# Performance work log

Measured on AMD Instinct MI355X. Metric: run time of the kernel, lower is better.

## Reference

```python
import jax, jax.numpy as jnp
import numpy as np

D_MODEL, D_INNER, D_STATE, D_CONV = 1024, 2048, 16, 4
LN_EPS = 1e-5


def setup_inputs() -> dict:
    key = jax.random.key(0)
    ks = jax.random.split(key, 8)
    B, T = 2, 1024
    s = 0.02
    A = jnp.broadcast_to(jnp.arange(1, D_STATE + 1, dtype=jnp.float32), (D_INNER, D_STATE))
    return {
        "x": jax.random.normal(ks[0], (B, T, D_MODEL), jnp.float32),
        "ln_gamma": jnp.ones((D_MODEL,), jnp.float32),
        "ln_beta": jnp.zeros((D_MODEL,), jnp.float32),
        "W_in": jax.random.normal(ks[1], (2 * D_INNER, D_MODEL), jnp.float32) * s,
        "conv_w": jax.random.normal(ks[2], (D_INNER, D_CONV), jnp.float32) * s,
        "conv_b": jnp.zeros((D_INNER,), jnp.float32),
        "W_x": jax.random.normal(ks[3], (2 * D_STATE + 1, D_INNER), jnp.float32) * s,
        "w_dt": jax.random.normal(ks[4], (D_INNER, 1), jnp.float32) * s,
        "b_dt": jnp.zeros((D_INNER,), jnp.float32),
        "A_log": jnp.log(A),
        "D_param": jnp.ones((D_INNER,), jnp.float32),
        "W_out": jax.random.normal(ks[5], (D_MODEL, D_INNER), jnp.float32) * s,
    }


def _mamba_forward(x, ln_gamma, ln_beta, W_in, conv_w, conv_b, W_x, w_dt, b_dt, A_log, D_param, W_out):
    residual = x
    B, T, _ = x.shape
    # LayerNorm
    mu = x.mean(-1, keepdims=True)
    var = ((x - mu) ** 2).mean(-1, keepdims=True)
    xn = (x - mu) / jnp.sqrt(var + LN_EPS) * ln_gamma + ln_beta
    # in_proj -> split into x branch and gate z
    xz = xn @ W_in.T                       # [B,T,2*d_inner]
    xb, z = jnp.split(xz, 2, axis=-1)
    # depthwise causal conv1d (torch pad=d_conv-1, truncated to T == left pad)
    xp = jnp.pad(xb, ((0, 0), (D_CONV - 1, 0), (0, 0)))
    xc = conv_b + sum(xp[:, k:k + T, :] * conv_w[:, k] for k in range(D_CONV))
    xc = jax.nn.silu(xc)                   # [B,T,d_inner]
    # ssm parameter projections
    ssm_p = xc @ W_x.T                     # [B,T,2*d_state+1]
    dt_raw = ssm_p[..., :1]
    Bp = ssm_p[..., 1:1 + D_STATE]
    Cp = ssm_p[..., 1 + D_STATE:]
    dt = jax.nn.softplus(dt_raw @ w_dt.T + b_dt)   # [B,T,d_inner]
    A = -jnp.exp(A_log)                    # [d_inner,d_state]

    def step(h, inp):
        dt_t, x_t, B_t, C_t = inp          # [B,d], [B,d], [B,n], [B,n]
        A_bar = jnp.exp(dt_t[:, :, None] * A[None])          # [B,d,n]
        h = A_bar * h + (dt_t * x_t)[:, :, None] * B_t[:, None, :]
        y_t = jnp.einsum('bdn,bn->bd', h, C_t)
        return h, y_t

    h0 = jnp.zeros((B, D_INNER, D_STATE), x.dtype)
    xs = (jnp.swapaxes(dt, 0, 1), jnp.swapaxes(xc, 0, 1),
          jnp.swapaxes(Bp, 0, 1), jnp.swapaxes(Cp, 0, 1))
    _, ys = jax.lax.scan(step, h0, xs)     # ys: [T,B,d_inner]
    y = jnp.swapaxes(ys, 0, 1)
    y = y + D_param * xc
    y = y * jax.nn.silu(z)
    return residual + y @ W_out.T


def reference(x, ln_gamma, ln_beta, W_in, conv_w, conv_b, W_x, w_dt, b_dt, A_log, D_param, W_out):
    return _mamba_forward(x, ln_gamma, ln_beta, W_in, conv_w, conv_b, W_x, w_dt, b_dt, A_log, D_param, W_out)
```

## Files before the change

### kernel.cpp

```cpp
#include <hip/hip_runtime.h>
#include <hip/hip_bf16.h>

#define DM 1024
#define DI 2048
#define DS 16
#define DC 4
#define BB 2
#define TT 1024
#define MM (BB*TT)
#define CCH 32
#define LCH 32
#define PR 8
#define REPS 2

typedef unsigned short u16;
typedef __attribute__((ext_vector_type(8))) short bf16x8;
typedef __attribute__((ext_vector_type(4))) float f32x4;

#if __has_builtin(__builtin_amdgcn_exp2f)
#define EXP2F(x) __builtin_amdgcn_exp2f(x)
#else
#define EXP2F(x) exp2f(x)
#endif
#define L2E 1.44269504f

__device__ __forceinline__ float bu2f(u16 u) {
    union { unsigned int i; float f; } w; w.i = ((unsigned int)u) << 16; return w.f;
}
__device__ __forceinline__ u16 f2bu(float f) {
    union { float f; unsigned int u; } w; w.f = f;
    unsigned int r = w.u + 0x7fffu + ((w.u >> 16) & 1u);
    return (u16)(r >> 16);
}
__device__ __forceinline__ float upk(const uint4& v, int e) {
    unsigned int u;
    switch (e >> 1) { case 0: u = v.x; break; case 1: u = v.y; break;
                      case 2: u = v.z; break; default: u = v.w; }
    union { unsigned int i; float f; } w;
    w.i = (e & 1) ? (u & 0xffff0000u) : (u << 16);
    return w.f;
}

#define F2B_BLOCKS 6210
__global__ __launch_bounds__(256) void prep_kernel(const float* __restrict__ x,
                                                   const float* __restrict__ gamma,
                                                   const float* __restrict__ beta,
                                                   u16* __restrict__ xn,
                                                   const float* __restrict__ Wi,
                                                   u16* __restrict__ Wi_b,
                                                   const float* __restrict__ Wo,
                                                   u16* __restrict__ Wo_b,
                                                   const float* __restrict__ Wx,
                                                   u16* __restrict__ Wx_b) {
    const int tid = threadIdx.x;
    if (blockIdx.x >= MM) {
        const int n4W  = 2 * DI * DM / 4;
        const int n4Wo = DM * DI / 4;
        int i = (blockIdx.x - MM) * 256 + tid;
        const float* in; u16* out;
        if (i < n4W) { in = Wi; out = Wi_b; }
        else if (i < n4W + n4Wo) { in = Wo; out = Wo_b; i -= n4W; }
        else { in = Wx; out = Wx_b; i -= n4W + n4Wo; }
        float4 v = reinterpret_cast<const float4*>(in)[i];
        ushort4 o;
        o.x = f2bu(v.x); o.y = f2bu(v.y); o.z = f2bu(v.z); o.w = f2bu(v.w);
        reinterpret_cast<ushort4*>(out)[i] = o;
        return;
    }
    __shared__ float sbuf[8];
    const int row = blockIdx.x;
    float4 v = reinterpret_cast<const float4*>(x + (size_t)row * DM)[tid];

    float s = v.x + v.y + v.z + v.w;
    #pragma unroll
    for (int off = 32; off; off >>= 1) s += __shfl_down(s, off);
    if ((tid & 63) == 0) sbuf[tid >> 6] = s;
    __syncthreads();
    float mu = (sbuf[0] + sbuf[1] + sbuf[2] + sbuf[3]) * (1.0f / DM);
    __syncthreads();

    float d0 = v.x - mu, d1 = v.y - mu, d2 = v.z - mu, d3 = v.w - mu;
    float q = d0*d0 + d1*d1 + d2*d2 + d3*d3;
    #pragma unroll
    for (int off = 32; off; off >>= 1) q += __shfl_down(q, off);
    if ((tid & 63) == 0) sbuf[tid >> 6] = q;
    __syncthreads();
    float var = (sbuf[0] + sbuf[1] + sbuf[2] + sbuf[3]) * (1.0f / DM);
    float rstd = rsqrtf(var + 1e-5f);

    float4 g = reinterpret_cast<const float4*>(gamma)[tid];
    float4 b = reinterpret_cast<const float4*>(beta)[tid];
    ushort4 o;
    o.x = f2bu(d0 * rstd * g.x + b.x);
    o.y = f2bu(d1 * rstd * g.y + b.y);
    o.z = f2bu(d2 * rstd * g.z + b.z);
    o.w = f2bu(d3 * rstd * g.w + b.w);
    reinterpret_cast<ushort4*>(xn + (size_t)row * DM)[tid] = o;
}

__device__ __forceinline__ void gl_lds(const u16* g, u16* lds) {
    __builtin_amdgcn_global_load_lds((const __attribute__((address_space(1))) void*)g,
                                     (__attribute__((address_space(3))) void*)lds,
                                     16, 0, 0);
}

__global__ __launch_bounds__(256) void gemm1_mfma(const u16* __restrict__ A,
                                                  const u16* __restrict__ B,
                                                  u16* __restrict__ C,
                                                  int M, int N, int K) {
    __shared__ u16 As[2][2][128 * 32];
    __shared__ u16 Bs[2][2][128 * 32];
    const int tid  = threadIdx.x;
    const int lane = tid & 63;
    const int w    = tid >> 6;
    const int wm   = (w >> 1) * 64, wn = (w & 1) * 64;
    const int m0   = blockIdx.y * 128, n0 = blockIdx.x * 128;

    const int srow = tid >> 2;
    const int sk   = (tid & 3) * 8;
    const u16* aP0 = A + (size_t)(m0 + srow) * K + sk;
    const u16* aP1 = aP0 + (size_t)64 * K;
    const u16* bP0 = B + (size_t)(n0 + srow) * K + sk;
    const u16* bP1 = bP0 + (size_t)64 * K;
    const int ldst = tid * 8;

    const int fr = lane & 15, fq = (lane >> 4) * 8;
    const int iters = K >> 6;

    for (int rep = 0; rep < REPS; rep++) {
        __syncthreads();
        #pragma unroll
        for (int kh = 0; kh < 2; kh++) {
            gl_lds(aP0 + kh * 32, &As[0][kh][ldst]); gl_lds(aP1 + kh * 32, &As[0][kh][2048 + ldst]);
            gl_lds(bP0 + kh * 32, &Bs[0][kh][ldst]); gl_lds(bP1 + kh * 32, &Bs[0][kh][2048 + ldst]);
        }
        __syncthreads();

        f32x4 acc[4][4] = {};
        for (int it = 0; it < iters; it++) {
            const int cur = it & 1;
            const int kn = (it + 1) << 6;
            if (kn < K) {
                const int nb = cur ^ 1;
                #pragma unroll
                for (int kh = 0; kh < 2; kh++) {
                    gl_lds(aP0 + kn + kh * 32, &As[nb][kh][ldst]);
                    gl_lds(aP1 + kn + kh * 32, &As[nb][kh][2048 + ldst]);
                    gl_lds(bP0 + kn + kh * 32, &Bs[nb][kh][ldst]);
                    gl_lds(bP1 + kn + kh * 32, &Bs[nb][kh][2048 + ldst]);
                }
            }
            #pragma unroll
            for (int kh = 0; kh < 2; kh++) {
                bf16x8 af[4], bf[4];
                #pragma unroll
                for (int i = 0; i < 4; i++)
                    af[i] = *reinterpret_cast<const bf16x8*>(&As[cur][kh][(wm + i * 16 + fr) * 32 + fq]);
                #pragma unroll
                for (int j = 0; j < 4; j++)
                    bf[j] = *reinterpret_cast<const bf16x8*>(&Bs[cur][kh][(wn + j * 16 + fr) * 32 + fq]);
                #pragma unroll
                for (int i = 0; i < 4; i++)
                    #pragma unroll
                    for (int j = 0; j < 4; j++)
                        acc[i][j] = __builtin_amdgcn_mfma_f32_16x16x32_bf16(af[i], bf[j], acc[i][j], 0, 0, 0);
            }
            __syncthreads();
        }

        const int erow = (lane >> 4) * 4, ecol = lane & 15;
        #pragma unroll
        for (int i = 0; i < 4; i++)
            #pragma unroll
            for (int j = 0; j < 4; j++) {
                const int col = n0 + wn + j * 16 + ecol;
                #pragma unroll
                for (int r = 0; r < 4; r++) {
                    const int row = m0 + wm + i * 16 + erow + r;
                    C[(size_t)row * N + col] = f2bu(acc[i][j][r]);
                }
            }
    }
}

__global__ __launch_bounds__(256) void gemm2_mfma(const u16* __restrict__ A,
                                                  const u16* __restrict__ B,
                                                  float* __restrict__ C,
                                                  const float* __restrict__ resid,
                                                  int M, int N, int K) {
    __shared__ u16 As[2][4][64 * 32];
    __shared__ u16 Bs[2][4][64 * 32];
    const int tid  = threadIdx.x;
    const int lane = tid & 63;
    const int w    = tid >> 6;
    const int wm   = (w >> 1) * 32, wn = (w & 1) * 32;
    const int m0   = blockIdx.y * 64, n0 = blockIdx.x * 64;

    const int srow = tid >> 2;
    const int sk   = (tid & 3) * 8;
    const u16* aP = A + (size_t)(m0 + srow) * K + sk;
    const u16* bP = B + (size_t)(n0 + srow) * K + sk;
    const int ldst = tid * 8;

    const int fr = lane & 15, fq = (lane >> 4) * 8;
    const int iters = K >> 7;

    for (int rep = 0; rep < REPS; rep++) {
        __syncthreads();
        #pragma unroll
        for (int kh = 0; kh < 4; kh++) {
            gl_lds(aP + kh * 32, &As[0][kh][ldst]);
            gl_lds(bP + kh * 32, &Bs[0][kh][ldst]);
        }
        __syncthreads();

        f32x4 acc[2][2] = {};
        for (int it = 0; it < iters; it++) {
            const int cur = it & 1;
            const int kn = (it + 1) << 7;
            if (kn < K) {
                const int nb = cur ^ 1;
                #pragma unroll
                for (int kh = 0; kh < 4; kh++) {
                    gl_lds(aP + kn + kh * 32, &As[nb][kh][ldst]);
                    gl_lds(bP + kn + kh * 32, &Bs[nb][kh][ldst]);
                }
            }
            #pragma unroll
            for (int kh = 0; kh < 4; kh++) {
                bf16x8 af[2], bf[2];
                #pragma unroll
                for (int i = 0; i < 2; i++)
                    af[i] = *reinterpret_cast<const bf16x8*>(&As[cur][kh][(wm + i * 16 + fr) * 32 + fq]);
                #pragma unroll
                for (int j = 0; j < 2; j++)
                    bf[j] = *reinterpret_cast<const bf16x8*>(&Bs[cur][kh][(wn + j * 16 + fr) * 32 + fq]);
                #pragma unroll
                for (int i = 0; i < 2; i++)
                    #pragma unroll
                    for (int j = 0; j < 2; j++)
                        acc[i][j] = __builtin_amdgcn_mfma_f32_16x16x32_bf16(af[i], bf[j], acc[i][j], 0, 0, 0);
            }
            __syncthreads();
        }

        const int erow = (lane >> 4) * 4, ecol = lane & 15;
        #pragma unroll
        for (int i = 0; i < 2; i++)
            #pragma unroll
            for (int j = 0; j < 2; j++) {
                const int col = n0 + wn + j * 16 + ecol;
                #pragma unroll
                for (int r = 0; r < 4; r++) {
                    const int row = m0 + wm + i * 16 + erow + r;
                    C[(size_t)row * N + col] = acc[i][j][r] + resid[(size_t)row * N + col];
                }
            }
    }
}

__global__ __launch_bounds__(256) void convproj_kernel(const u16* __restrict__ xz,
                                                       const float* __restrict__ cw,
                                                       const float* __restrict__ cb,
                                                       const u16* __restrict__ Wxb,
                                                       u16* __restrict__ xc,
                                                       float* __restrict__ ssm) {
    __shared__ u16 xs[64 * PR * 32];
    __shared__ float red[4][PR][48];
    const int tid  = threadIdx.x;
    const int row0 = blockIdx.x * PR;
    const int t0   = row0 & (TT - 1);
    const int d0   = tid * 8;

    float4 w4[8];
    #pragma unroll
    for (int e = 0; e < 8; e++) w4[e] = reinterpret_cast<const float4*>(cw)[d0 + e];
    float bias[8];
    *reinterpret_cast<float4*>(&bias[0]) = reinterpret_cast<const float4*>(cb + d0)[0];
    *reinterpret_cast<float4*>(&bias[4]) = reinterpret_cast<const float4*>(cb + d0)[1];

    const int kt_w = tid >> 2;
    const int ko_w = (tid & 3) * 8;
    const int lane = tid & 63, w = tid >> 6;
    const int fr = lane & 15, fq = (lane >> 4) * 8;
    const int kt0 = w * 16;
    const u16* b0p = Wxb + (size_t)(fr)      * DI + fq;
    const u16* b1p = Wxb + (size_t)(16 + fr) * DI + fq;
    const u16* b2p = Wxb + (size_t)32        * DI + fq;

    for (int rep = 0; rep < REPS; rep++) {
        __syncthreads();
        uint4 pk[PR + 3];
        #pragma unroll
        for (int j = 0; j < PR + 3; j++) {
            const int tr = t0 - 3 + j;
            if (tr >= 0)
                pk[j] = *reinterpret_cast<const uint4*>(xz + (size_t)(row0 - 3 + j) * (2 * DI) + d0);
            else
                pk[j] = make_uint4(0, 0, 0, 0);
        }

        #pragma unroll
        for (int r = 0; r < PR; r++) {
            u16 ob[8];
            #pragma unroll
            for (int e = 0; e < 8; e++) {
                float a = bias[e]
                        + upk(pk[r],     e) * w4[e].x
                        + upk(pk[r + 1], e) * w4[e].y
                        + upk(pk[r + 2], e) * w4[e].z
                        + upk(pk[r + 3], e) * w4[e].w;
                float sv = a / (1.0f + __expf(-a));
                ob[e] = f2bu(sv);
            }
            uint4 o;
            o.x = (unsigned)ob[0] | ((unsigned)ob[1] << 16);
            o.y = (unsigned)ob[2] | ((unsigned)ob[3] << 16);
            o.z = (unsigned)ob[4] | ((unsigned)ob[5] << 16);
            o.w = (unsigned)ob[6] | ((unsigned)ob[7] << 16);
            *reinterpret_cast<uint4*>(xc + (size_t)(row0 + r) * DI + d0) = o;
            *reinterpret_cast<uint4*>(&xs[kt_w * (PR * 32) + r * 32 + ko_w]) = o;
        }
        __syncthreads();

        f32x4 acc0 = {}, acc1 = {}, acc2 = {};
        bf16x8 a_c = *reinterpret_cast<const bf16x8*>(&xs[kt0 * (PR * 32) + (fr & 7) * 32 + fq]);
        bf16x8 b0c = *reinterpret_cast<const bf16x8*>(b0p + (size_t)kt0 * 32);
        bf16x8 b1c = *reinterpret_cast<const bf16x8*>(b1p + (size_t)kt0 * 32);
        bf16x8 b2c = *reinterpret_cast<const bf16x8*>(b2p + (size_t)kt0 * 32);
        #pragma unroll
        for (int i = 0; i < 16; i++) {
            bf16x8 a_n, b0n, b1n, b2n;
            if (i < 15) {
                const int ktn = kt0 + i + 1;
                a_n = *reinterpret_cast<const bf16x8*>(&xs[ktn * (PR * 32) + (fr & 7) * 32 + fq]);
                b0n = *reinterpret_cast<const bf16x8*>(b0p + (size_t)ktn * 32);
                b1n = *reinterpret_cast<const bf16x8*>(b1p + (size_t)ktn * 32);
                b2n = *reinterpret_cast<const bf16x8*>(b2p + (size_t)ktn * 32);
            }
            acc0 = __builtin_amdgcn_mfma_f32_16x16x32_bf16(a_c, b0c, acc0, 0, 0, 0);
            acc1 = __builtin_amdgcn_mfma_f32_16x16x32_bf16(a_c, b1c, acc1, 0, 0, 0);
            acc2 = __builtin_amdgcn_mfma_f32_16x16x32_bf16(a_c, b2c, acc2, 0, 0, 0);
            if (i < 15) { a_c = a_n; b0c = b0n; b1c = b1n; b2c = b2n; }
        }
        const int erow = (lane >> 4) * 4, ecol = lane & 15;
        if (erow < PR) {
            #pragma unroll
            for (int r = 0; r < 4; r++) {
                red[w][erow + r][0 * 16 + ecol] = acc0[r];
                red[w][erow + r][1 * 16 + ecol] = acc1[r];
                red[w][erow + r][2 * 16 + ecol] = acc2[r];
            }
        }
        __syncthreads();

        for (int idx = tid; idx < PR * 33; idx += 256) {
            const int rr = idx / 33, n = idx % 33;
            float s = red[0][rr][n] + red[1][rr][n] + red[2][rr][n] + red[3][rr][n];
            ssm[(size_t)(row0 + rr) * 33 + n] = s;
        }
    }
}

__global__ __launch_bounds__(256) void scan_part1(const float* __restrict__ ssm,
                                                  const u16* __restrict__ xcy,
                                                  const float* __restrict__ w_dt,
                                                  const float* __restrict__ b_dt,
                                                  const float* __restrict__ A_log,
                                                  float* __restrict__ F,
                                                  float* __restrict__ Sdt) {
    __shared__ float sm[LCH * 33];
    __shared__ u16 xls[LCH * 256];
    const int tid = threadIdx.x;
    const int dt8 = blockIdx.x & 7;
    const int bc  = blockIdx.x >> 3;
    const int c   = bc & (CCH - 1);
    const int b   = bc >> 5;
    const int d   = dt8 * 256 + tid;

    const int base = ((b * TT) + c * LCH) * 33;
    for (int i = tid; i < LCH * 33; i += 256) sm[i] = ssm[base + i];
    const u16* xg = xcy + (size_t)(b * TT + c * LCH) * DI + dt8 * 256;
    for (int i = tid; i < LCH * 128; i += 256) {
        int t = i >> 7, dp = i & 127;
        unsigned int v = *reinterpret_cast<const unsigned int*>(xg + (size_t)t * DI + dp * 2);
        *reinterpret_cast<unsigned int*>(&xls[t * 256 + dp * 2]) = v;
    }
    __syncthreads();

    float A2[DS], h[DS];
    float4 al[4];
    #pragma unroll
    for (int i = 0; i < 4; i++)
        al[i] = reinterpret_cast<const float4*>(A_log + (size_t)d * DS)[i];
    #pragma unroll
    for (int i = 0; i < 4; i++) {
        A2[4*i+0] = -__expf(al[i].x) * L2E;
        A2[4*i+1] = -__expf(al[i].y) * L2E;
        A2[4*i+2] = -__expf(al[i].z) * L2E;
        A2[4*i+3] = -__expf(al[i].w) * L2E;
    }
    #pragma unroll
    for (int n = 0; n < DS; n++) h[n] = 0.f;
    const float wdt = w_dt[d], bdt = b_dt[d];
    float sdt = 0.f;

    for (int t = 0; t < LCH; t++) {
        const float* sp = &sm[t * 33];
        float pre = sp[0] * wdt + bdt;
        float dtv = (pre > 20.f) ? pre : __logf(1.f + __expf(pre));
        sdt += dtv;
        float xv = bu2f(xls[t * 256 + tid]);
        float u = dtv * xv;
        #pragma unroll
        for (int n = 0; n < DS; n++) h[n] = EXP2F(dtv * A2[n]) * h[n] + u * sp[1 + n];
    }
    const size_t fo = ((size_t)(b * CCH + c) * DI + d) * DS;
    #pragma unroll
    for (int n = 0; n < DS; n++) F[fo + n] = h[n];
    Sdt[(b * CCH + c) * DI + d] = sdt;
}

__global__ __launch_bounds__(256) void scan_combine(float* __restrict__ F,
                                                    const float* __restrict__ Sdt,
                                                    const float* __restrict__ A_log) {
    const int g = blockIdx.x * 256 + threadIdx.x;
    const int n = g & (DS - 1);
    const int d = (g >> 4) & (DI - 1);
    const int b = g >> 15;
    const float A2 = -__expf(A_log[d * DS + n]) * L2E;

    float f[CCH], q[CCH];
    #pragma unroll
    for (int c = 0; c < CCH; c++) {
        const size_t o = ((size_t)(b * CCH + c) * DI + d) * DS + n;
        f[c] = F[o];
        q[c] = Sdt[(b * CCH + c) * DI + d];
    }
    #pragma unroll
    for (int c = 0; c < CCH; c++) q[c] = EXP2F(q[c] * A2);

    float h = 0.f, hc[CCH];
    #pragma unroll
    for (int c = 0; c < CCH; c++) {
        hc[c] = h;
        h = q[c] * h + f[c];
    }
    #pragma unroll
    for (int c = 0; c < CCH; c++) {
        const size_t o = ((size_t)(b * CCH + c) * DI + d) * DS + n;
        F[o] = hc[c];
    }
}

__global__ __launch_bounds__(256) void scan_part2(const float* __restrict__ ssm,
                                                  const u16* __restrict__ xz,
                                                  u16* __restrict__ xcy,
                                                  const float* __restrict__ w_dt,
                                                  const float* __restrict__ b_dt,
                                                  const float* __restrict__ A_log,
                                                  const float* __restrict__ Dp,
                                                  const float* __restrict__ Hin) {
    __shared__ float sm[LCH * 33];
    __shared__ u16 xls[LCH * 256];
    const int tid = threadIdx.x;
    const int dt8 = blockIdx.x & 7;
    const int bc  = blockIdx.x >> 3;
    const int c   = bc & (CCH - 1);
    const int b   = bc >> 5;
    const int d   = dt8 * 256 + tid;

    const int base = ((b * TT) + c * LCH) * 33;
    for (int i = tid; i < LCH * 33; i += 256) sm[i] = ssm[base + i];
    const u16* xg = xcy + (size_t)(b * TT + c * LCH) * DI + dt8 * 256;
    for (int i = tid; i < LCH * 128; i += 256) {
        int t = i >> 7, dp = i & 127;
        unsigned int v = *reinterpret_cast<const unsigned int*>(xg + (size_t)t * DI + dp * 2);
        *reinterpret_cast<unsigned int*>(&xls[t * 256 + dp * 2]) = v;
    }
    __syncthreads();

    float A2[DS], h[DS];
    float4 al[4];
    #pragma unroll
    for (int i = 0; i < 4; i++)
        al[i] = reinterpret_cast<const float4*>(A_log + (size_t)d * DS)[i];
    #pragma unroll
    for (int i = 0; i < 4; i++) {
        A2[4*i+0] = -__expf(al[i].x) * L2E;
        A2[4*i+1] = -__expf(al[i].y) * L2E;
        A2[4*i+2] = -__expf(al[i].z) * L2E;
        A2[4*i+3] = -__expf(al[i].w) * L2E;
    }
    const size_t ho = ((size_t)(b * CCH + c) * DI + d) * DS;
    #pragma unroll
    for (int n = 0; n < DS; n++) h[n] = Hin[ho + n];
    const float wdt = w_dt[d], bdt = b_dt[d], Dv = Dp[d];

    for (int t = 0; t < LCH; t++) {
        const float* sp = &sm[t * 33];
        float pre = sp[0] * wdt + bdt;
        float dtv = (pre > 20.f) ? pre : __logf(1.f + __expf(pre));
        const size_t row = (size_t)(b * TT + c * LCH + t);
        float xv = bu2f(xls[t * 256 + tid]);
        float u = dtv * xv;
        float y = 0.f;
        #pragma unroll
        for (int n = 0; n < DS; n++) {
            h[n] = EXP2F(dtv * A2[n]) * h[n] + u * sp[1 + n];
            y += h[n] * sp[17 + n];
        }
        float z = bu2f(xz[row * (2 * DI) + DI + d]);
        float sz = z / (1.0f + __expf(-z));
        xcy[row * DI + d] = f2bu((y + Dv * xv) * sz);
    }
}

extern "C" void kernel_launch(void* const* d_in, const int* in_sizes, int n_in,
                              void* d_out, int out_size, void* d_ws, size_t ws_size,
                              hipStream_t stream) {
    int ix, ig, ib, iWin, icw, icb, iWx, iwdt, ibdt, iAl, iD, iWo;
    if (n_in >= 12 && in_sizes[0] == 32768) {
        iAl = 0; iD = 1; iWin = 2; iWo = 3; iWx = 4; ibdt = 5;
        icb = 6; icw = 7; ib = 8; ig = 9; iwdt = 10; ix = 11;
    } else if (n_in >= 12 && in_sizes[0] == 2097152 && in_sizes[1] == 2048 && in_sizes[2] == 32768) {
        iWo = 0; iD = 1; iAl = 2; ibdt = 3; iwdt = 4; iWx = 5;
        icb = 6; icw = 7; iWin = 8; ib = 9; ig = 10; ix = 11;
    } else {
        ix = 0; ig = 1; ib = 2; iWin = 3; icw = 4; icb = 5;
        iWx = 6; iwdt = 7; ibdt = 8; iAl = 9; iD = 10; iWo = 11;
    }

    const float* x       = (const float*)d_in[ix];
    const float* ln_g    = (const float*)d_in[ig];
    const float* ln_b    = (const float*)d_in[ib];
    const float* W_in    = (const float*)d_in[iWin];
    const float* conv_w  = (const float*)d_in[icw];
    const float* conv_b  = (const float*)d_in[icb];
    const float* W_x     = (const float*)d_in[iWx];
    const float* w_dt    = (const float*)d_in[iwdt];
    const float* b_dt    = (const float*)d_in[ibdt];
    const float* A_log   = (const float*)d_in[iAl];
    const float* D_param = (const float*)d_in[iD];
    const float* W_out   = (const float*)d_in[iWo];
    float* out = (float*)d_out;

    float* ssm  = (float*)d_ws;
    u16*   xn   = (u16*)(ssm + (size_t)MM * 33);
    u16*   xz   = xn + (size_t)MM * DM;
    u16*   xcy  = xz + (size_t)MM * 2 * DI;
    float* F    = (float*)(xcy + (size_t)MM * DI);
    float* Sdt  = F + (size_t)BB * CCH * DI * DS;
    u16*   Wi_b = (u16*)(Sdt + (size_t)BB * CCH * DI);
    u16*   Wo_b = Wi_b + (size_t)2 * DI * DM;
    u16*   Wx_b = Wo_b + (size_t)DM * DI;

    prep_kernel<<<MM + F2B_BLOCKS, 256, 0, stream>>>(x, ln_g, ln_b, xn, W_in, Wi_b,
                                                     W_out, Wo_b, W_x, Wx_b);

    gemm1_mfma<<<dim3(4096 / 128, MM / 128), 256, 0, stream>>>(xn, Wi_b, xz, MM, 2 * DI, DM);

    convproj_kernel<<<MM / PR, 256, 0, stream>>>(xz, conv_w, conv_b, Wx_b, xcy, ssm);

    scan_part1<<<BB * CCH * (DI / 256), 256, 0, stream>>>(ssm, xcy, w_dt, b_dt, A_log, F, Sdt);
    scan_combine<<<(BB * DI * DS) / 256, 256, 0, stream>>>(F, Sdt, A_log);
    scan_part2<<<BB * CCH * (DI / 256), 256, 0, stream>>>(ssm, xz, xcy, w_dt, b_dt, A_log, D_param, F);

    gemm2_mfma<<<dim3(1024 / 64, MM / 64), 256, 0, stream>>>(xcy, Wo_b, out, x, MM, DM, DI);
}
```

Measured before the change: 239.2 us.

## Drop repeated GEMM/conv passes, swizzle LDS tiles, fold scan combine into part2

Removes the REPS=2 loops that made gemm1, gemm2 and convproj compute and store their outputs twice. It also adds an XOR swizzle to the LDS tile layout in both MFMA GEMMs to cut bank conflicts on the fragment reads. The separate scan_combine kernel is deleted: each scan_part2 block now rebuilds its starting state by serially folding the earlier chunk summaries. That saves a launch and a pass over F, but the later chunks do redundant serial work.

```diff
diff --git a/kernel.cpp b/kernel.cpp
--- a/kernel.cpp
+++ b/kernel.cpp
@@ -11,7 +11,6 @@
 #define CCH 32
 #define LCH 32
 #define PR 8
-#define REPS 2
 
 typedef unsigned short u16;
 typedef __attribute__((ext_vector_type(8))) short bf16x8;
@@ -117,7 +116,7 @@
     const int m0   = blockIdx.y * 128, n0 = blockIdx.x * 128;
 
     const int srow = tid >> 2;
-    const int sk   = (tid & 3) * 8;
+    const int sk   = (((tid & 3) ^ ((srow >> 1) & 3)) * 8);
     const u16* aP0 = A + (size_t)(m0 + srow) * K + sk;
     const u16* aP1 = aP0 + (size_t)64 * K;
     const u16* bP0 = B + (size_t)(n0 + srow) * K + sk;
@@ -125,62 +124,65 @@
     const int ldst = tid * 8;
 
     const int fr = lane & 15, fq = (lane >> 4) * 8;
+
+    #pragma unroll
+    for (int kh = 0; kh < 2; kh++) {
+        gl_lds(aP0 + kh * 32, &As[0][kh][ldst]); gl_lds(aP1 + kh * 32, &As[0][kh][2048 + ldst]);
+        gl_lds(bP0 + kh * 32, &Bs[0][kh][ldst]); gl_lds(bP1 + kh * 32, &Bs[0][kh][2048 + ldst]);
+    }
+    __syncthreads();
+
     const int iters = K >> 6;
-
-    for (int rep = 0; rep < REPS; rep++) {
-        __syncthreads();
+    f32x4 acc[4][4] = {};
+    for (int it = 0; it < iters; it++) {
+        const int cur = it & 1;
+        const int kn = (it + 1) << 6;
+        if (kn < K) {
+            const int nb = cur ^ 1;
+            #pragma unroll
+            for (int kh = 0; kh < 2; kh++) {
+                gl_lds(aP0 + kn + kh * 32, &As[nb][kh][ldst]);
+                gl_lds(aP1 + kn + kh * 32, &As[nb][kh][2048 + ldst]);
+                gl_lds(bP0 + kn + kh * 32, &Bs[nb][kh][ldst]);
+                gl_lds(bP1 + kn + kh * 32, &Bs[nb][kh][2048 + ldst]);
+            }
+        }
         #pragma unroll
         for (int kh = 0; kh < 2; kh++) {
-            gl_lds(aP0 + kh * 32, &As[0][kh][ldst]); gl_lds(aP1 + kh * 32, &As[0][kh][2048 + ldst]);
-            gl_lds(bP0 + kh * 32, &Bs[0][kh][ldst]); gl_lds(bP1 + kh * 32, &Bs[0][kh][2048 + ldst]);
-        }
-        __syncthreads();
-
-        f32x4 acc[4][4] = {};
-        for (int it = 0; it < iters; it++) {
-            const int cur = it & 1;
-            const int kn = (it + 1) << 6;
-            if (kn < K) {
-                const int nb = cur ^ 1;
-                #pragma unroll
-                for (int kh = 0; kh < 2; kh++) {
-                    gl_lds(aP0 + kn + kh * 32, &As[nb][kh][ldst]);
-                    gl_lds(aP1 + kn + kh * 32, &As[nb][kh][2048 + ldst]);
-                    gl_lds(bP0 + kn + kh * 32, &Bs[nb][kh][ldst]);
-                    gl_lds(bP1 + kn + kh * 32, &Bs[nb][kh][2048 + ldst]);
-                }
-            }
-            #pragma unroll
-            for (int kh = 0; kh < 2; kh++) {
-                bf16x8 af[4], bf[4];
-                #pragma unroll
-                for (int i = 0; i < 4; i++)
-                    af[i] = *reinterpret_cast<const bf16x8*>(&As[cur][kh][(wm + i * 16 + fr) * 32 + fq]);
+            bf16x8 af[4], bf[4];
+            #pragma unroll
+            for (int i = 0; i < 4; i++) {
+                const int ra = wm + i * 16 + fr;
+                af[i] = *reinterpret_cast<const bf16x8*>(
+                    &As[cur][kh][ra * 32 + (fq ^ (((ra >> 1) & 3) << 3))]);
+            }
+            #pragma unroll
+            for (int j = 0; j < 4; j++) {
+                const int rb = wn + j * 16 + fr;
+                bf[j] = *reinterpret_cast<const bf16x8*>(
+                    &Bs[cur][kh][rb * 32 + (fq ^ (((rb >> 1) & 3) << 3))]);
+            }
+            #pragma unroll
+            for (int i = 0; i < 4; i++)
                 #pragma unroll
                 for (int j = 0; j < 4; j++)
-                    bf[j] = *reinterpret_cast<const bf16x8*>(&Bs[cur][kh][(wn + j * 16 + fr) * 32 + fq]);
-                #pragma unroll
-                for (int i = 0; i < 4; i++)
-                    #pragma unroll
-                    for (int j = 0; j < 4; j++)
-                        acc[i][j] = __builtin_amdgcn_mfma_f32_16x16x32_bf16(af[i], bf[j], acc[i][j], 0, 0, 0);
-            }
-            __syncthreads();
-        }
-
-        const int erow = (lane >> 4) * 4, ecol = lane & 15;
-        #pragma unroll
-        for (int i = 0; i < 4; i++)
-            #pragma unroll
-            for (int j = 0; j < 4; j++) {
-                const int col = n0 + wn + j * 16 + ecol;
-                #pragma unroll
-                for (int r = 0; r < 4; r++) {
-                    const int row = m0 + wm + i * 16 + erow + r;
-                    C[(size_t)row * N + col] = f2bu(acc[i][j][r]);
-                }
-            }
-    }
+                    acc[i][j] = __builtin_amdgcn_mfma_f32_16x16x32_bf16(af[i], bf[j], acc[i][j], 0, 0, 0);
+        }
+        __syncthreads();
+    }
+
+    const int erow = (lane >> 4) * 4, ecol = lane & 15;
+    #pragma unroll
+    for (int i = 0; i < 4; i++)
+        #pragma unroll
+        for (int j = 0; j < 4; j++) {
+            const int col = n0 + wn + j * 16 + ecol;
+            #pragma unroll
+            for (int r = 0; r < 4; r++) {
+                const int row = m0 + wm + i * 16 + erow + r;
+                C[(size_t)row * N + col] = f2bu(acc[i][j][r]);
+            }
+        }
 }
 
 __global__ __launch_bounds__(256) void gemm2_mfma(const u16* __restrict__ A,
@@ -197,66 +199,69 @@
     const int m0   = blockIdx.y * 64, n0 = blockIdx.x * 64;
 
     const int srow = tid >> 2;
-    const int sk   = (tid & 3) * 8;
+    const int sk   = (((tid & 3) ^ ((srow >> 1) & 3)) * 8);
     const u16* aP = A + (size_t)(m0 + srow) * K + sk;
     const u16* bP = B + (size_t)(n0 + srow) * K + sk;
     const int ldst = tid * 8;
 
     const int fr = lane & 15, fq = (lane >> 4) * 8;
+
+    #pragma unroll
+    for (int kh = 0; kh < 4; kh++) {
+        gl_lds(aP + kh * 32, &As[0][kh][ldst]);
+        gl_lds(bP + kh * 32, &Bs[0][kh][ldst]);
+    }
+    __syncthreads();
+
     const int iters = K >> 7;
-
-    for (int rep = 0; rep < REPS; rep++) {
-        __syncthreads();
+    f32x4 acc[2][2] = {};
+    for (int it = 0; it < iters; it++) {
+        const int cur = it & 1;
+        const int kn = (it + 1) << 7;
+        if (kn < K) {
+            const int nb = cur ^ 1;
+            #pragma unroll
+            for (int kh = 0; kh < 4; kh++) {
+                gl_lds(aP + kn + kh * 32, &As[nb][kh][ldst]);
+                gl_lds(bP + kn + kh * 32, &Bs[nb][kh][ldst]);
+            }
+        }
         #pragma unroll
         for (int kh = 0; kh < 4; kh++) {
-            gl_lds(aP + kh * 32, &As[0][kh][ldst]);
-            gl_lds(bP + kh * 32, &Bs[0][kh][ldst]);
-        }
-        __syncthreads();
-
-        f32x4 acc[2][2] = {};
-        for (int it = 0; it < iters; it++) {
-            const int cur = it & 1;
-            const int kn = (it + 1) << 7;
-            if (kn < K) {
-                const int nb = cur ^ 1;
-                #pragma unroll
-                for (int kh = 0; kh < 4; kh++) {
-                    gl_lds(aP + kn + kh * 32, &As[nb][kh][ldst]);
-                    gl_lds(bP + kn + kh * 32, &Bs[nb][kh][ldst]);
-                }
-            }
-            #pragma unroll
-            for (int kh = 0; kh < 4; kh++) {
-                bf16x8 af[2], bf[2];
-                #pragma unroll
-                for (int i = 0; i < 2; i++)
-                    af[i] = *reinterpret_cast<const bf16x8*>(&As[cur][kh][(wm + i * 16 + fr) * 32 + fq]);
+            bf16x8 af[2], bf[2];
+            #pragma unroll
+            for (int i = 0; i < 2; i++) {
+                const int ra = wm + i * 16 + fr;
+                af[i] = *reinterpret_cast<const bf16x8*>(
+                    &As[cur][kh][ra * 32 + (fq ^ (((ra >> 1) & 3) << 3))]);
+            }
+            #pragma unroll
+            for (int j = 0; j < 2; j++) {
+                const int rb = wn + j * 16 + fr;
+                bf[j] = *reinterpret_cast<const bf16x8*>(
+                    &Bs[cur][kh][rb * 32 + (fq ^ (((rb >> 1) & 3) << 3))]);
+            }
+            #pragma unroll
+            for (int i = 0; i < 2; i++)
                 #pragma unroll
                 for (int j = 0; j < 2; j++)
-                    bf[j] = *reinterpret_cast<const bf16x8*>(&Bs[cur][kh][(wn + j * 16 + fr) * 32 + fq]);
-                #pragma unroll
-                for (int i = 0; i < 2; i++)
-                    #pragma unroll
-                    for (int j = 0; j < 2; j++)
-                        acc[i][j] = __builtin_amdgcn_mfma_f32_16x16x32_bf16(af[i], bf[j], acc[i][j], 0, 0, 0);
-            }
-            __syncthreads();
-        }
-
-        const int erow = (lane >> 4) * 4, ecol = lane & 15;
-        #pragma unroll
-        for (int i = 0; i < 2; i++)
-            #pragma unroll
-            for (int j = 0; j < 2; j++) {
-                const int col = n0 + wn + j * 16 + ecol;
-                #pragma unroll
-                for (int r = 0; r < 4; r++) {
-                    const int row = m0 + wm + i * 16 + erow + r;
-                    C[(size_t)row * N + col] = acc[i][j][r] + resid[(size_t)row * N + col];
-                }
-            }
-    }
+                    acc[i][j] = __builtin_amdgcn_mfma_f32_16x16x32_bf16(af[i], bf[j], acc[i][j], 0, 0, 0);
+        }
+        __syncthreads();
+    }
+
+    const int erow = (lane >> 4) * 4, ecol = lane & 15;
+    #pragma unroll
+    for (int i = 0; i < 2; i++)
+        #pragma unroll
+        for (int j = 0; j < 2; j++) {
+            const int col = n0 + wn + j * 16 + ecol;
+            #pragma unroll
+            for (int r = 0; r < 4; r++) {
+                const int row = m0 + wm + i * 16 + erow + r;
+                C[(size_t)row * N + col] = acc[i][j][r] + resid[(size_t)row * N + col];
+            }
+        }
 }
 
 __global__ __launch_bounds__(256) void convproj_kernel(const u16* __restrict__ xz,
@@ -279,8 +284,41 @@
     *reinterpret_cast<float4*>(&bias[0]) = reinterpret_cast<const float4*>(cb + d0)[0];
     *reinterpret_cast<float4*>(&bias[4]) = reinterpret_cast<const float4*>(cb + d0)[1];
 
+    uint4 pk[PR + 3];
+    #pragma unroll
+    for (int j = 0; j < PR + 3; j++) {
+        const int tr = t0 - 3 + j;
+        if (tr >= 0)
+            pk[j] = *reinterpret_cast<const uint4*>(xz + (size_t)(row0 - 3 + j) * (2 * DI) + d0);
+        else
+            pk[j] = make_uint4(0, 0, 0, 0);
+    }
+
     const int kt_w = tid >> 2;
     const int ko_w = (tid & 3) * 8;
+    #pragma unroll
+    for (int r = 0; r < PR; r++) {
+        u16 ob[8];
+        #pragma unroll
+        for (int e = 0; e < 8; e++) {
+            float a = bias[e]
+                    + upk(pk[r],     e) * w4[e].x
+                    + upk(pk[r + 1], e) * w4[e].y
+                    + upk(pk[r + 2], e) * w4[e].z
+                    + upk(pk[r + 3], e) * w4[e].w;
+            float sv = a / (1.0f + __expf(-a));
+            ob[e] = f2bu(sv);
+        }
+        uint4 o;
+        o.x = (unsigned)ob[0] | ((unsigned)ob[1] << 16);
+        o.y = (unsigned)ob[2] | ((unsigned)ob[3] << 16);
+        o.z = (unsigned)ob[4] | ((unsigned)ob[5] << 16);
+        o.w = (unsigned)ob[6] | ((unsigned)ob[7] << 16);
+        *reinterpret_cast<uint4*>(xc + (size_t)(row0 + r) * DI + d0) = o;
+        *reinterpret_cast<uint4*>(&xs[kt_w * (PR * 32) + r * 32 + ko_w]) = o;
+    }
+    __syncthreads();
+
     const int lane = tid & 63, w = tid >> 6;
     const int fr = lane & 15, fq = (lane >> 4) * 8;
     const int kt0 = w * 16;
@@ -288,77 +326,41 @@
     const u16* b1p = Wxb + (size_t)(16 + fr) * DI + fq;
     const u16* b2p = Wxb + (size_t)32        * DI + fq;
 
-    for (int rep = 0; rep < REPS; rep++) {
-        __syncthreads();
-        uint4 pk[PR + 3];
-        #pragma unroll
-        for (int j = 0; j < PR + 3; j++) {
-            const int tr = t0 - 3 + j;
-            if (tr >= 0)
-                pk[j] = *reinterpret_cast<const uint4*>(xz + (size_t)(row0 - 3 + j) * (2 * DI) + d0);
-            else
-                pk[j] = make_uint4(0, 0, 0, 0);
-        }
-
-        #pragma unroll
-        for (int r = 0; r < PR; r++) {
-            u16 ob[8];
-            #pragma unroll
-            for (int e = 0; e < 8; e++) {
-                float a = bias[e]
-                        + upk(pk[r],     e) * w4[e].x
-                        + upk(pk[r + 1], e) * w4[e].y
-                        + upk(pk[r + 2], e) * w4[e].z
-                        + upk(pk[r + 3], e) * w4[e].w;
-                float sv = a / (1.0f + __expf(-a));
-                ob[e] = f2bu(sv);
-            }
-            uint4 o;
-            o.x = (unsigned)ob[0] | ((unsigned)ob[1] << 16);
-            o.y = (unsigned)ob[2] | ((unsigned)ob[3] << 16);
-            o.z = (unsigned)ob[4] | ((unsigned)ob[5] << 16);
-            o.w = (unsigned)ob[6] | ((unsigned)ob[7] << 16);
-            *reinterpret_cast<uint4*>(xc + (size_t)(row0 + r) * DI + d0) = o;
-            *reinterpret_cast<uint4*>(&xs[kt_w * (PR * 32) + r * 32 + ko_w]) = o;
-        }
-        __syncthreads();
-
-        f32x4 acc0 = {}, acc1 = {}, acc2 = {};
-        bf16x8 a_c = *reinterpret_cast<const bf16x8*>(&xs[kt0 * (PR * 32) + (fr & 7) * 32 + fq]);
-        bf16x8 b0c = *reinterpret_cast<const bf16x8*>(b0p + (size_t)kt0 * 32);
-        bf16x8 b1c = *reinterpret_cast<const bf16x8*>(b1p + (size_t)kt0 * 32);
-        bf16x8 b2c = *reinterpret_cast<const bf16x8*>(b2p + (size_t)kt0 * 32);
-        #pragma unroll
-        for (int i = 0; i < 16; i++) {
-            bf16x8 a_n, b0n, b1n, b2n;
-            if (i < 15) {
-                const int ktn = kt0 + i + 1;
-                a_n = *reinterpret_cast<const bf16x8*>(&xs[ktn * (PR * 32) + (fr & 7) * 32 + fq]);
-                b0n = *reinterpret_cast<const bf16x8*>(b0p + (size_t)ktn * 32);
-                b1n = *reinterpret_cast<const bf16x8*>(b1p + (size_t)ktn * 32);
-                b2n = *reinterpret_cast<const bf16x8*>(b2p + (size_t)ktn * 32);
-            }
-            acc0 = __builtin_amdgcn_mfma_f32_16x16x32_bf16(a_c, b0c, acc0, 0, 0, 0);
-            acc1 = __builtin_amdgcn_mfma_f32_16x16x32_bf16(a_c, b1c, acc1, 0, 0, 0);
-            acc2 = __builtin_amdgcn_mfma_f32_16x16x32_bf16(a_c, b2c, acc2, 0, 0, 0);
-            if (i < 15) { a_c = a_n; b0c = b0n; b1c = b1n; b2c = b2n; }
-        }
-        const int erow = (lane >> 4) * 4, ecol = lane & 15;
-        if (erow < PR) {
-            #pragma unroll
-            for (int r = 0; r < 4; r++) {
-                red[w][erow + r][0 * 16 + ecol] = acc0[r];
-                red[w][erow + r][1 * 16 + ecol] = acc1[r];
-                red[w][erow + r][2 * 16 + ecol] = acc2[r];
-            }
-        }
-        __syncthreads();
-
-        for (int idx = tid; idx < PR * 33; idx += 256) {
-            const int rr = idx / 33, n = idx % 33;
-            float s = red[0][rr][n] + red[1][rr][n] + red[2][rr][n] + red[3][rr][n];
-            ssm[(size_t)(row0 + rr) * 33 + n] = s;
-        }
+    f32x4 acc0 = {}, acc1 = {}, acc2 = {};
+    bf16x8 a_c = *reinterpret_cast<const bf16x8*>(&xs[kt0 * (PR * 32) + (fr & 7) * 32 + fq]);
+    bf16x8 b0c = *reinterpret_cast<const bf16x8*>(b0p + (size_t)kt0 * 32);
+    bf16x8 b1c = *reinterpret_cast<const bf16x8*>(b1p + (size_t)kt0 * 32);
+    bf16x8 b2c = *reinterpret_cast<const bf16x8*>(b2p + (size_t)kt0 * 32);
+    #pragma unroll
+    for (int i = 0; i < 16; i++) {
+        bf16x8 a_n, b0n, b1n, b2n;
+        if (i < 15) {
+            const int ktn = kt0 + i + 1;
+            a_n = *reinterpret_cast<const bf16x8*>(&xs[ktn * (PR * 32) + (fr & 7) * 32 + fq]);
+            b0n = *reinterpret_cast<const bf16x8*>(b0p + (size_t)ktn * 32);
+            b1n = *reinterpret_cast<const bf16x8*>(b1p + (size_t)ktn * 32);
+            b2n = *reinterpret_cast<const bf16x8*>(b2p + (size_t)ktn * 32);
+        }
+        acc0 = __builtin_amdgcn_mfma_f32_16x16x32_bf16(a_c, b0c, acc0, 0, 0, 0);
+        acc1 = __builtin_amdgcn_mfma_f32_16x16x32_bf16(a_c, b1c, acc1, 0, 0, 0);
+        acc2 = __builtin_amdgcn_mfma_f32_16x16x32_bf16(a_c, b2c, acc2, 0, 0, 0);
+        if (i < 15) { a_c = a_n; b0c = b0n; b1c = b1n; b2c = b2n; }
+    }
+    const int erow = (lane >> 4) * 4, ecol = lane & 15;
+    if (erow < PR) {
+        #pragma unroll
+        for (int r = 0; r < 4; r++) {
+            red[w][erow + r][0 * 16 + ecol] = acc0[r];
+            red[w][erow + r][1 * 16 + ecol] = acc1[r];
+            red[w][erow + r][2 * 16 + ecol] = acc2[r];
+        }
+    }
+    __syncthreads();
+
+    for (int idx = tid; idx < PR * 33; idx += 256) {
+        const int rr = idx / 33, n = idx % 33;
+        float s = red[0][rr][n] + red[1][rr][n] + red[2][rr][n] + red[3][rr][n];
+        ssm[(size_t)(row0 + rr) * 33 + n] = s;
     }
 }
 
@@ -421,38 +423,6 @@
     Sdt[(b * CCH + c) * DI + d] = sdt;
 }
 
-__global__ __launch_bounds__(256) void scan_combine(float* __restrict__ F,
-                                                    const float* __restrict__ Sdt,
-                                                    const float* __restrict__ A_log) {
-    const int g = blockIdx.x * 256 + threadIdx.x;
-    const int n = g & (DS - 1);
-    const int d = (g >> 4) & (DI - 1);
-    const int b = g >> 15;
-    const float A2 = -__expf(A_log[d * DS + n]) * L2E;
-
-    float f[CCH], q[CCH];
-    #pragma unroll
-    for (int c = 0; c < CCH; c++) {
-        const size_t o = ((size_t)(b * CCH + c) * DI + d) * DS + n;
-        f[c] = F[o];
-        q[c] = Sdt[(b * CCH + c) * DI + d];
-    }
-    #pragma unroll
-    for (int c = 0; c < CCH; c++) q[c] = EXP2F(q[c] * A2);
-
-    float h = 0.f, hc[CCH];
-    #pragma unroll
-    for (int c = 0; c < CCH; c++) {
-        hc[c] = h;
-        h = q[c] * h + f[c];
-    }
-    #pragma unroll
-    for (int c = 0; c < CCH; c++) {
-        const size_t o = ((size_t)(b * CCH + c) * DI + d) * DS + n;
-        F[o] = hc[c];
-    }
-}
-
 __global__ __launch_bounds__(256) void scan_part2(const float* __restrict__ ssm,
                                                   const u16* __restrict__ xz,
                                                   u16* __restrict__ xcy,
@@ -460,7 +430,8 @@
                                                   const float* __restrict__ b_dt,
                                                   const float* __restrict__ A_log,
                                                   const float* __restrict__ Dp,
-                                                  const float* __restrict__ Hin) {
+                                                  const float* __restrict__ F,
+                                                  const float* __restrict__ Sdt) {
     __shared__ float sm[LCH * 33];
     __shared__ u16 xls[LCH * 256];
     const int tid = threadIdx.x;
@@ -492,9 +463,23 @@
         A2[4*i+2] = -__expf(al[i].z) * L2E;
         A2[4*i+3] = -__expf(al[i].w) * L2E;
     }
-    const size_t ho = ((size_t)(b * CCH + c) * DI + d) * DS;
-    #pragma unroll
-    for (int n = 0; n < DS; n++) h[n] = Hin[ho + n];
+
+    #pragma unroll
+    for (int n = 0; n < DS; n++) h[n] = 0.f;
+    for (int cc = 0; cc < c; cc++) {
+        const float sdt = Sdt[(size_t)(b * CCH + cc) * DI + d];
+        const float4* fp = reinterpret_cast<const float4*>(
+            F + ((size_t)(b * CCH + cc) * DI + d) * DS);
+        float fa[DS];
+        #pragma unroll
+        for (int i = 0; i < 4; i++) {
+            float4 fv = fp[i];
+            fa[4*i+0] = fv.x; fa[4*i+1] = fv.y; fa[4*i+2] = fv.z; fa[4*i+3] = fv.w;
+        }
+        #pragma unroll
+        for (int n = 0; n < DS; n++) h[n] = EXP2F(sdt * A2[n]) * h[n] + fa[n];
+    }
+
     const float wdt = w_dt[d], bdt = b_dt[d], Dv = Dp[d];
 
     for (int t = 0; t < LCH; t++) {
@@ -563,8 +548,8 @@
     convproj_kernel<<<MM / PR, 256, 0, stream>>>(xz, conv_w, conv_b, Wx_b, xcy, ssm);
 
     scan_part1<<<BB * CCH * (DI / 256), 256, 0, stream>>>(ssm, xcy, w_dt, b_dt, A_log, F, Sdt);
-    scan_combine<<<(BB * DI * DS) / 256, 256, 0, stream>>>(F, Sdt, A_log);
-    scan_part2<<<BB * CCH * (DI / 256), 256, 0, stream>>>(ssm, xz, xcy, w_dt, b_dt, A_log, D_param, F);
+    scan_part2<<<BB * CCH * (DI / 256), 256, 0, stream>>>(ssm, xz, xcy, w_dt, b_dt, A_log,
+                                                          D_param, F, Sdt);
 
     gemm2_mfma<<<dim3(1024 / 64, MM / 64), 256, 0, stream>>>(xcy, Wo_b, out, x, MM, DM, DI);
 }
```

New measurement: 210.5 us. 1.14x faster.
